# Performance work log

Measured on AMD Instinct MI355X. Metric: run time of the kernel, lower is better.

Reference implementation:

```python
import jax, jax.numpy as jnp
import numpy as np

H = 12      # num_attention_heads
D = 768     # hidden_size
DK = D // H # per-head dim


def setup_inputs() -> dict:
    key = jax.random.key(0)
    ks = jax.random.split(key, 8)
    B, S = 2, 4096
    scale = 0.02
    return {
        "query": jax.random.normal(ks[0], (B, S, D), jnp.float32),
        "key": jax.random.normal(ks[1], (B, S, D), jnp.float32),
        "value": jax.random.normal(ks[2], (B, S, D), jnp.float32),
        "mask": jnp.ones((B, S), jnp.float32),
        "Wq": jax.random.normal(ks[3], (D, D), jnp.float32) * scale,
        "bq": jnp.zeros((D,), jnp.float32),
        "Wk": jax.random.normal(ks[4], (D, D), jnp.float32) * scale,
        "bk": jnp.zeros((D,), jnp.float32),
        "Wv": jax.random.normal(ks[5], (D, D), jnp.float32) * scale,
        "bv": jnp.zeros((D,), jnp.float32),
    }


def reference(query, key, value, mask, Wq, bq, Wk, bk, Wv, bv):
    B, Sq, _ = query.shape
    Sk = key.shape[1]
    # attention mask: ones[B,Sq,1] * mask[B,1,Sk] -> [B,Sq,Sk] -> [B,1,Sq,Sk]
    attn_mask = jnp.ones((B, Sq, 1), jnp.float32) * mask[:, None, :]
    adder = (1.0 - attn_mask)[:, None, :, :] * -10000.0

    q = (query @ Wq + bq).reshape(B, Sq, H, DK).transpose(0, 2, 1, 3)  # [B,H,Sq,DK]
    k = (key @ Wk + bk).reshape(B, Sk, H, DK).transpose(0, 2, 1, 3)
    v = (value @ Wv + bv).reshape(B, Sk, H, DK).transpose(0, 2, 1, 3)

    scores = jnp.einsum("bhqd,bhkd->bhqk", q, k) / jnp.sqrt(jnp.float32(DK))
    scores = scores + adder
    probs = jax.nn.softmax(scores, axis=-1)  # dropout inactive (training=False)
    out = jnp.einsum("bhqk,bhkd->bhqd", probs, v)
    return out.transpose(0, 2, 1, 3).reshape(B, Sq, D)
```

## Files before the change

### kernel.cpp

```cpp
#include <hip/hip_runtime.h>
#include <stdint.h>

#define NH 12
#define DMODEL 768
#define HDK 64
#define SEQ 4096
#define NB 2

typedef __attribute__((ext_vector_type(8))) short bf16x8;
typedef __attribute__((ext_vector_type(4))) short s16x4;
typedef __attribute__((ext_vector_type(4))) float f32x4;
typedef __attribute__((ext_vector_type(16))) float f32x16;

#define LOG2E 1.44269504f
#define QSCALE 0.18033688f
#define CSUB 4.0f

__device__ __forceinline__ unsigned short f2bf(float x) {
    union { float f; unsigned u; } v; v.f = x;
    unsigned r = v.u + 0x7FFFu + ((v.u >> 16) & 1u);
    return (unsigned short)(r >> 16);
}

__device__ __forceinline__ unsigned pack2bf(float a, float b) {
    union { float f; unsigned u; } x, y; x.f = a; y.f = b;
    return __builtin_amdgcn_perm(y.u + 0x8000u, x.u + 0x8000u, 0x07060302u);
}

__device__ __forceinline__ unsigned pack2bf_t(float a, float b) {
    union { float f; unsigned u; } x, y; x.f = a; y.f = b;
    return __builtin_amdgcn_perm(y.u, x.u, 0x07060302u);
}

__device__ __forceinline__ void lds_dma16(const void* g, void* l) {
    __builtin_amdgcn_global_load_lds(
        (const __attribute__((address_space(1))) void*)g,
        (__attribute__((address_space(3))) void*)l, 16, 0, 0);
}

__global__ __launch_bounds__(256) void wt_kernel(
    const float* __restrict__ Wq, const float* __restrict__ Wk,
    const float* __restrict__ Wv, unsigned short* __restrict__ Wt) {
    __shared__ float ts[32][33];
    int mat = blockIdx.z;
    const float* W = (mat == 0) ? Wq : ((mat == 1) ? Wk : Wv);
    unsigned short* out = Wt + (size_t)mat * DMODEL * DMODEL;
    int k0 = blockIdx.x * 32;
    int n0 = blockIdx.y * 32;
    int t = threadIdx.x;
    int row = t >> 3, c4 = (t & 7) * 4;
    float4 v = *(const float4*)&W[(size_t)(k0 + row) * DMODEL + n0 + c4];
    ts[row][c4 + 0] = v.x; ts[row][c4 + 1] = v.y;
    ts[row][c4 + 2] = v.z; ts[row][c4 + 3] = v.w;
    __syncthreads();
    s16x4 o;
    o[0] = (short)f2bf(ts[c4 + 0][row]);
    o[1] = (short)f2bf(ts[c4 + 1][row]);
    o[2] = (short)f2bf(ts[c4 + 2][row]);
    o[3] = (short)f2bf(ts[c4 + 3][row]);
    *(s16x4*)&out[(size_t)(n0 + row) * DMODEL + k0 + c4] = o;
}

__global__ __launch_bounds__(256) void qkv_gemm4(
    const float* __restrict__ Aq, const float* __restrict__ Ak,
    const float* __restrict__ Av, const unsigned short* __restrict__ Wt,
    const float* __restrict__ bq, const float* __restrict__ bk,
    const float* __restrict__ bv,
    unsigned short* __restrict__ Qw, unsigned short* __restrict__ Kw,
    unsigned short* __restrict__ Vt) {
    __shared__ float As[128 * 64];
    __shared__ unsigned short Bs[128 * 64];
    int mat = blockIdx.z;
    const float* A = (mat == 0) ? Aq : ((mat == 1) ? Ak : Av);
    const unsigned short* W = Wt + (size_t)mat * DMODEL * DMODEL;
    const float* bias = (mat == 0) ? bq : ((mat == 1) ? bk : bv);
    int m0 = blockIdx.x * 128;
    int n0 = blockIdx.y * 128;
    int tid = threadIdx.x;
    int lane = tid & 63, wv = tid >> 6;
    int wm = (wv & 1) * 64, wn = (wv >> 1) * 64;
    int lm = lane & 15, quad = lane >> 4;

    const float* aS[8];
    float* aD[8];
    #pragma unroll
    for (int i = 0; i < 8; ++i) {
        int g = i * 256 + tid;
        int R = g >> 4, S = g & 15, c = (S & 8) | ((S & 7) ^ (R & 7));
        aS[i] = A + (size_t)(m0 + R) * DMODEL + c * 4;
        aD[i] = &As[(i * 256 + wv * 64) * 4];
    }
    const unsigned short* bS[4];
    unsigned short* bD[4];
    #pragma unroll
    for (int i = 0; i < 4; ++i) {
        int g = i * 256 + tid;
        int R = g >> 3, S = g & 7, c = S ^ (R & 7);
        bS[i] = W + (size_t)(n0 + R) * DMODEL + c * 8;
        bD[i] = &Bs[(i * 256 + wv * 64) * 8];
    }

    f32x4 acc[4][4] = {};
    int sx = lm & 7;
    const bool swapC = (mat < 2);
    for (int kt = 0; kt < 12; ++kt) {
        __syncthreads();
        #pragma unroll
        for (int i = 0; i < 8; ++i) lds_dma16(aS[i], aD[i]);
        #pragma unroll
        for (int i = 0; i < 4; ++i) lds_dma16(bS[i], bD[i]);
        #pragma unroll
        for (int i = 0; i < 8; ++i) aS[i] += 64;
        #pragma unroll
        for (int i = 0; i < 4; ++i) bS[i] += 64;
        __syncthreads();
        #pragma unroll
        for (int ks = 0; ks < 2; ++ks) {
            bf16x8 af[4], bfr[4];
            #pragma unroll
            for (int i = 0; i < 4; ++i) {
                int r = wm + i * 16 + lm;
                int c0 = ks * 8 + quad * 2;
                int s0 = (c0 & 8) | ((c0 & 7) ^ sx);
                int s1 = (c0 & 8) | (((c0 + 1) & 7) ^ sx);
                f32x4 lo = *(const f32x4*)&As[r * 64 + s0 * 4];
                f32x4 hi = *(const f32x4*)&As[r * 64 + s1 * 4];
                unsigned* au = (unsigned*)&af[i];
                au[0] = pack2bf(lo[0], lo[1]);
                au[1] = pack2bf(lo[2], lo[3]);
                au[2] = pack2bf(hi[0], hi[1]);
                au[3] = pack2bf(hi[2], hi[3]);
            }
            #pragma unroll
            for (int j = 0; j < 4; ++j)
                bfr[j] = *(const bf16x8*)&Bs[(wn + j * 16 + lm) * 64 +
                                             (((ks * 4 + quad) ^ sx) << 3)];
            if (swapC) {
                #pragma unroll
                for (int i = 0; i < 4; ++i)
                    #pragma unroll
                    for (int j = 0; j < 4; ++j)
                        acc[i][j] = __builtin_amdgcn_mfma_f32_16x16x32_bf16(
                            bfr[j], af[i], acc[i][j], 0, 0, 0);
            } else {
                #pragma unroll
                for (int i = 0; i < 4; ++i)
                    #pragma unroll
                    for (int j = 0; j < 4; ++j)
                        acc[i][j] = __builtin_amdgcn_mfma_f32_16x16x32_bf16(
                            af[i], bfr[j], acc[i][j], 0, 0, 0);
            }
        }
    }
    if (swapC) {
        float sc = (mat == 0) ? QSCALE : 1.0f;
        unsigned short* outp = (mat == 0) ? Qw : Kw;
        #pragma unroll
        for (int j = 0; j < 4; ++j) {
            int nbase = n0 + wn + j * 16 + quad * 4;
            f32x4 bvv = *(const f32x4*)&bias[nbase];
            int h = nbase >> 6, dk = nbase & 63;
            #pragma unroll
            for (int i = 0; i < 4; ++i) {
                int s = m0 + wm + i * 16 + lm;
                int b = s >> 12, ss = s & 4095;
                s16x4 o;
                #pragma unroll
                for (int r = 0; r < 4; ++r)
                    o[r] = (short)f2bf((acc[i][j][r] + bvv[r]) * sc);
                *(s16x4*)&outp[((size_t)(b * NH + h) * SEQ + ss) * HDK + dk] = o;
            }
        }
    } else {
        #pragma unroll
        for (int j = 0; j < 4; ++j) {
            int n = n0 + wn + j * 16 + lm;
            float bvv = bias[n];
            int h = n >> 6, dk = n & 63;
            #pragma unroll
            for (int i = 0; i < 4; ++i) {
                int mg = m0 + wm + i * 16 + quad * 4;
                int b = mg >> 12, s = mg & 4095;
                s16x4 o;
                #pragma unroll
                for (int r = 0; r < 4; ++r) o[r] = (short)f2bf(acc[i][j][r] + bvv);
                *(s16x4*)&Vt[((size_t)(b * NH + h) * HDK + dk) * SEQ + s] = o;
            }
        }
    }
}

__global__ __launch_bounds__(256, 3) void attn_kernel(
    const unsigned short* __restrict__ Qw, const unsigned short* __restrict__ Kw,
    const unsigned short* __restrict__ Vt, const float* __restrict__ mask,
    float* __restrict__ out) {
    __shared__ unsigned short Ks[128 * 64];
    __shared__ unsigned short Vs[64 * 128];
    __shared__ float adds[128];

    int q0 = blockIdx.x * 128;
    int bh = blockIdx.y;
    int b = bh / NH, h = bh % NH;
    const unsigned short* Qb = Qw + (size_t)bh * SEQ * HDK;
    const unsigned short* Kb = Kw + (size_t)bh * SEQ * HDK;
    const unsigned short* Vb = Vt + (size_t)bh * HDK * SEQ;
    const float* mb = mask + (size_t)b * SEQ;
    int tid = threadIdx.x;
    int lane = tid & 63, wv = tid >> 6;
    int L31 = lane & 31, hh = lane >> 5;

    int qrow = q0 + wv * 32 + L31;
    bf16x8 qf[4];
    #pragma unroll
    for (int t = 0; t < 4; ++t)
        qf[t] = *(const bf16x8*)&Qb[(size_t)qrow * HDK + t * 16 + hh * 8];

    const unsigned short* kS[4];
    const unsigned short* vS[4];
    unsigned short* kD[4];
    unsigned short* vD[4];
    #pragma unroll
    for (int i = 0; i < 4; ++i) {
        int cc = wv * 4 + i;
        {
            int rho = cc * 8 + (lane >> 3);
            int blk = rho >> 5, c = (rho >> 3) & 3, hb = (rho >> 2) & 1, r2 = rho & 3;
            int kc = blk * 32 + (c & 1) * 16 + hb * 8 + (c >> 1) * 4 + r2;
            int ch = (lane & 7) ^ (rho & 7);
            kS[i] = Kb + (size_t)kc * HDK + ch * 8;
            kD[i] = &Ks[cc * 512];
        }
        {
            int d = cc * 4 + (lane >> 4);
            int c = lane & 15;
            int ch = (c & 8) | ((c & 7) ^ (d & 7));
            vS[i] = Vb + (size_t)d * SEQ + ch * 8;
            vD[i] = &Vs[cc * 512];
        }
    }

    f32x16 Oacc[2] = {};
    f32x16 lacc = {};
    const f32x16 kZero = {};
    bf16x8 ones;
    #pragma unroll
    for (int i = 0; i < 8; ++i) ones[i] = (short)0x3F80;
    const int sx7 = L31 & 7;

    for (int kt = 0; kt < 32; ++kt) {
        __syncthreads();
        #pragma unroll
        for (int i = 0; i < 4; ++i) lds_dma16(kS[i], kD[i]);
        #pragma unroll
        for (int i = 0; i < 4; ++i) lds_dma16(vS[i], vD[i]);
        if (tid < 128)
            adds[tid] = ((1.0f - mb[kt * 128 + tid]) * -10000.0f - CSUB) * LOG2E;
        #pragma unroll
        for (int i = 0; i < 4; ++i) { kS[i] += 128 * HDK; vS[i] += 128; }
        __syncthreads();

        #pragma unroll
        for (int blk = 0; blk < 4; ++blk) {
            f32x16 sacc;
            {
                bf16x8 kf = *(const bf16x8*)&Ks[(blk * 32 + L31) * 64 +
                                                ((hh ^ sx7) << 3)];
                sacc = __builtin_amdgcn_mfma_f32_32x32x16_bf16(kf, qf[0], kZero, 0, 0, 0);
            }
            #pragma unroll
            for (int t = 1; t < 4; ++t) {
                bf16x8 kf = *(const bf16x8*)&Ks[(blk * 32 + L31) * 64 +
                                                (((2 * t + hh) ^ sx7) << 3)];
                sacc = __builtin_amdgcn_mfma_f32_32x32x16_bf16(kf, qf[t], sacc, 0, 0, 0);
            }

            unsigned pkk[2][4];
            #pragma unroll
            for (int c2 = 0; c2 < 4; ++c2) {
                f32x4 adv = *(const f32x4*)&adds[blk * 32 + (c2 & 1) * 16 +
                                                 (c2 >> 1) * 4 + hh * 8];
                float p0 = __builtin_amdgcn_exp2f(sacc[c2 * 4 + 0] + adv[0]);
                float p1 = __builtin_amdgcn_exp2f(sacc[c2 * 4 + 1] + adv[1]);
                float p2 = __builtin_amdgcn_exp2f(sacc[c2 * 4 + 2] + adv[2]);
                float p3 = __builtin_amdgcn_exp2f(sacc[c2 * 4 + 3] + adv[3]);
                pkk[c2 & 1][2 * (c2 >> 1) + 0] = pack2bf_t(p0, p1);
                pkk[c2 & 1][2 * (c2 >> 1) + 1] = pack2bf_t(p2, p3);
            }

            #pragma unroll
            for (int kbi = 0; kbi < 2; ++kbi) {
                bf16x8 pf;
                unsigned* pu = (unsigned*)&pf;
                pu[0] = pkk[kbi][0]; pu[1] = pkk[kbi][1];
                pu[2] = pkk[kbi][2]; pu[3] = pkk[kbi][3];
                int kb = blk * 2 + kbi;
                lacc = __builtin_amdgcn_mfma_f32_32x32x16_bf16(ones, pf, lacc, 0, 0, 0);
                #pragma unroll
                for (int dj = 0; dj < 2; ++dj) {
                    int c = kb * 2 + hh;
                    int slot = (c & 8) | ((c & 7) ^ (lane & 7));
                    bf16x8 vf = *(const bf16x8*)&Vs[(dj * 32 + L31) * 128 + slot * 8];
                    Oacc[dj] = __builtin_amdgcn_mfma_f32_32x32x16_bf16(vf, pf, Oacc[dj], 0, 0, 0);
                }
            }
        }
    }

    float rl = 1.0f / lacc[0];
    size_t base = ((size_t)b * SEQ + qrow) * DMODEL + h * HDK;
    #pragma unroll
    for (int dj = 0; dj < 2; ++dj)
        #pragma unroll
        for (int c2 = 0; c2 < 4; ++c2) {
            int d = dj * 32 + 8 * c2 + 4 * hh;
            float4 o;
            o.x = Oacc[dj][c2 * 4 + 0] * rl;
            o.y = Oacc[dj][c2 * 4 + 1] * rl;
            o.z = Oacc[dj][c2 * 4 + 2] * rl;
            o.w = Oacc[dj][c2 * 4 + 3] * rl;
            *(float4*)&out[base + d] = o;
        }
}

extern "C" void kernel_launch(void* const* d_in, const int* in_sizes, int n_in,
                              void* d_out, int out_size, void* d_ws, size_t ws_size,
                              hipStream_t stream) {
    (void)in_sizes; (void)n_in; (void)out_size; (void)ws_size;
    const float* query = (const float*)d_in[0];
    const float* key   = (const float*)d_in[1];
    const float* value = (const float*)d_in[2];
    const float* mask  = (const float*)d_in[3];
    const float* Wq    = (const float*)d_in[4];
    const float* bq    = (const float*)d_in[5];
    const float* Wk    = (const float*)d_in[6];
    const float* bk    = (const float*)d_in[7];
    const float* Wv    = (const float*)d_in[8];
    const float* bv    = (const float*)d_in[9];

    const size_t WT_BYTES  = (size_t)3 * DMODEL * DMODEL * 2;
    const size_t QKV_BYTES = (size_t)NB * NH * SEQ * HDK * 2;
    unsigned short* Wt = (unsigned short*)d_ws;
    unsigned short* Qw = (unsigned short*)((char*)d_ws + WT_BYTES);
    unsigned short* Kw = (unsigned short*)((char*)d_ws + WT_BYTES + QKV_BYTES);
    unsigned short* Vt = (unsigned short*)((char*)d_ws + WT_BYTES + 2 * QKV_BYTES);

    wt_kernel<<<dim3(24, 24, 3), 256, 0, stream>>>(Wq, Wk, Wv, Wt);
    qkv_gemm4<<<dim3(64, 6, 3), 256, 0, stream>>>(query, key, value, Wt,
                                                  bq, bk, bv, Qw, Kw, Vt);
    attn_kernel<<<dim3(32, 24), 256, 0, stream>>>(Qw, Kw, Vt, mask, (float*)d_out);
}
```

Measured before the change: 308.3 us.

## Restructure attention to 2-wave blocks with double-buffered K and swizzled grids

The attention kernel now uses 128-thread blocks where each wave handles 64 query rows as two 32-row tiles, sharing each K/V LDS fragment across two MFMA streams. K tiles are double-buffered so the next tile's DMA overlaps the current compute, with explicit waitcnt, barriers, sched_barrier and setprio around MFMA bursts. The row-sum is computed with scalar adds plus a cross-half shuffle instead of a ones-matrix MFMA. Both the GEMM and attention grids become 1D with an XCD-aware block swizzle. Risks include higher register pressure, lower occupancy from 2-wave blocks, and fragile hand-written vmcnt counts.

```diff
diff --git a/kernel.cpp b/kernel.cpp
--- a/kernel.cpp
+++ b/kernel.cpp
@@ -15,6 +15,8 @@
 #define LOG2E 1.44269504f
 #define QSCALE 0.18033688f
 #define CSUB 4.0f
+
+#define SBAR() __builtin_amdgcn_sched_barrier(0)
 
 __device__ __forceinline__ unsigned short f2bf(float x) {
     union { float f; unsigned u; } v; v.f = x;
@@ -70,12 +72,17 @@
     unsigned short* __restrict__ Vt) {
     __shared__ float As[128 * 64];
     __shared__ unsigned short Bs[128 * 64];
-    int mat = blockIdx.z;
+    int lin = blockIdx.x;
+    int swz = (lin & 7) * 144 + (lin >> 3);
+    int mat = swz / 384;
+    int rr = swz - mat * 384;
+    int mblk = rr / 6;
+    int nblk = rr - mblk * 6;
     const float* A = (mat == 0) ? Aq : ((mat == 1) ? Ak : Av);
     const unsigned short* W = Wt + (size_t)mat * DMODEL * DMODEL;
     const float* bias = (mat == 0) ? bq : ((mat == 1) ? bk : bv);
-    int m0 = blockIdx.x * 128;
-    int n0 = blockIdx.y * 128;
+    int m0 = mblk * 128;
+    int n0 = nblk * 128;
     int tid = threadIdx.x;
     int lane = tid & 63, wv = tid >> 6;
     int wm = (wv & 1) * 64, wn = (wv >> 1) * 64;
@@ -190,16 +197,18 @@
     }
 }
 
-__global__ __launch_bounds__(256, 3) void attn_kernel(
+__global__ __launch_bounds__(128, 2) void attn_kernel(
     const unsigned short* __restrict__ Qw, const unsigned short* __restrict__ Kw,
     const unsigned short* __restrict__ Vt, const float* __restrict__ mask,
     float* __restrict__ out) {
-    __shared__ unsigned short Ks[128 * 64];
+    __shared__ unsigned short Ks[2][128 * 64];
     __shared__ unsigned short Vs[64 * 128];
     __shared__ float adds[128];
 
-    int q0 = blockIdx.x * 128;
-    int bh = blockIdx.y;
+    int lin = blockIdx.x;
+    int swz = (lin & 7) * 96 + (lin >> 3);
+    int q0 = (swz & 31) * 128;
+    int bh = swz >> 5;
     int b = bh / NH, h = bh % NH;
     const unsigned short* Qb = Qw + (size_t)bh * SEQ * HDK;
     const unsigned short* Kb = Kw + (size_t)bh * SEQ * HDK;
@@ -208,117 +217,167 @@
     int tid = threadIdx.x;
     int lane = tid & 63, wv = tid >> 6;
     int L31 = lane & 31, hh = lane >> 5;
-
-    int qrow = q0 + wv * 32 + L31;
-    bf16x8 qf[4];
-    #pragma unroll
-    for (int t = 0; t < 4; ++t)
-        qf[t] = *(const bf16x8*)&Qb[(size_t)qrow * HDK + t * 16 + hh * 8];
-
-    const unsigned short* kS[4];
-    const unsigned short* vS[4];
-    unsigned short* kD[4];
-    unsigned short* vD[4];
-    #pragma unroll
-    for (int i = 0; i < 4; ++i) {
-        int cc = wv * 4 + i;
+    const int sx7 = L31 & 7;
+
+    int qrow = q0 + wv * 64 + L31;
+    bf16x8 qa[4], qbv[4];
+    #pragma unroll
+    for (int t = 0; t < 4; ++t) {
+        qa[t] = *(const bf16x8*)&Qb[(size_t)qrow * HDK + t * 16 + hh * 8];
+        qbv[t] = *(const bf16x8*)&Qb[(size_t)(qrow + 32) * HDK + t * 16 + hh * 8];
+    }
+    asm volatile("s_waitcnt vmcnt(0)" ::: "memory");
+
+    const unsigned short* kS[8];
+    const unsigned short* vS[8];
+    #pragma unroll
+    for (int i = 0; i < 8; ++i) {
+        int cc = wv * 8 + i;
         {
             int rho = cc * 8 + (lane >> 3);
             int blk = rho >> 5, c = (rho >> 3) & 3, hb = (rho >> 2) & 1, r2 = rho & 3;
             int kc = blk * 32 + (c & 1) * 16 + hb * 8 + (c >> 1) * 4 + r2;
             int ch = (lane & 7) ^ (rho & 7);
             kS[i] = Kb + (size_t)kc * HDK + ch * 8;
-            kD[i] = &Ks[cc * 512];
         }
         {
             int d = cc * 4 + (lane >> 4);
             int c = lane & 15;
             int ch = (c & 8) | ((c & 7) ^ (d & 7));
             vS[i] = Vb + (size_t)d * SEQ + ch * 8;
-            vD[i] = &Vs[cc * 512];
-        }
-    }
-
-    f32x16 Oacc[2] = {};
-    f32x16 lacc = {};
+        }
+    }
+    #pragma unroll
+    for (int i = 0; i < 8; ++i) {
+        lds_dma16(kS[i], &Ks[0][(wv * 8 + i) * 512]);
+        kS[i] += 128 * HDK;
+    }
+    SBAR();
+
+    f32x16 Oa[2] = {}, Ob[2] = {};
+    float lpa = 0.0f, lpb = 0.0f;
     const f32x16 kZero = {};
-    bf16x8 ones;
-    #pragma unroll
-    for (int i = 0; i < 8; ++i) ones[i] = (short)0x3F80;
-    const int sx7 = L31 & 7;
 
     for (int kt = 0; kt < 32; ++kt) {
-        __syncthreads();
-        #pragma unroll
-        for (int i = 0; i < 4; ++i) lds_dma16(kS[i], kD[i]);
-        #pragma unroll
-        for (int i = 0; i < 4; ++i) lds_dma16(vS[i], vD[i]);
-        if (tid < 128)
-            adds[tid] = ((1.0f - mb[kt * 128 + tid]) * -10000.0f - CSUB) * LOG2E;
-        #pragma unroll
-        for (int i = 0; i < 4; ++i) { kS[i] += 128 * HDK; vS[i] += 128; }
-        __syncthreads();
+        int cur = kt & 1;
+        const unsigned short* Kc = &Ks[cur][0];
+        SBAR();
+        __builtin_amdgcn_s_barrier();
+        SBAR();
+        float mbv = mb[kt * 128 + tid];
+        adds[tid] = ((1.0f - mbv) * -10000.0f - CSUB) * LOG2E;
+        SBAR();
+        #pragma unroll
+        for (int i = 0; i < 8; ++i) {
+            lds_dma16(vS[i], &Vs[(wv * 8 + i) * 512]);
+            vS[i] += 128;
+        }
+        if (kt < 31) {
+            unsigned short* kn = &Ks[cur ^ 1][0];
+            #pragma unroll
+            for (int i = 0; i < 8; ++i) {
+                lds_dma16(kS[i], kn + (wv * 8 + i) * 512);
+                kS[i] += 128 * HDK;
+            }
+        }
+        SBAR();
+        asm volatile("s_waitcnt lgkmcnt(0)" ::: "memory");
+        __builtin_amdgcn_s_barrier();
+        SBAR();
 
         #pragma unroll
         for (int blk = 0; blk < 4; ++blk) {
-            f32x16 sacc;
+            f32x16 sa, sb;
+            __builtin_amdgcn_s_setprio(1);
             {
-                bf16x8 kf = *(const bf16x8*)&Ks[(blk * 32 + L31) * 64 +
+                bf16x8 kf = *(const bf16x8*)&Kc[(blk * 32 + L31) * 64 +
                                                 ((hh ^ sx7) << 3)];
-                sacc = __builtin_amdgcn_mfma_f32_32x32x16_bf16(kf, qf[0], kZero, 0, 0, 0);
+                sa = __builtin_amdgcn_mfma_f32_32x32x16_bf16(kf, qa[0], kZero, 0, 0, 0);
+                sb = __builtin_amdgcn_mfma_f32_32x32x16_bf16(kf, qbv[0], kZero, 0, 0, 0);
             }
             #pragma unroll
             for (int t = 1; t < 4; ++t) {
-                bf16x8 kf = *(const bf16x8*)&Ks[(blk * 32 + L31) * 64 +
+                bf16x8 kf = *(const bf16x8*)&Kc[(blk * 32 + L31) * 64 +
                                                 (((2 * t + hh) ^ sx7) << 3)];
-                sacc = __builtin_amdgcn_mfma_f32_32x32x16_bf16(kf, qf[t], sacc, 0, 0, 0);
-            }
-
-            unsigned pkk[2][4];
+                sa = __builtin_amdgcn_mfma_f32_32x32x16_bf16(kf, qa[t], sa, 0, 0, 0);
+                sb = __builtin_amdgcn_mfma_f32_32x32x16_bf16(kf, qbv[t], sb, 0, 0, 0);
+            }
+            __builtin_amdgcn_s_setprio(0);
+
+            unsigned pkkA[2][4], pkkB[2][4];
             #pragma unroll
             for (int c2 = 0; c2 < 4; ++c2) {
                 f32x4 adv = *(const f32x4*)&adds[blk * 32 + (c2 & 1) * 16 +
                                                  (c2 >> 1) * 4 + hh * 8];
-                float p0 = __builtin_amdgcn_exp2f(sacc[c2 * 4 + 0] + adv[0]);
-                float p1 = __builtin_amdgcn_exp2f(sacc[c2 * 4 + 1] + adv[1]);
-                float p2 = __builtin_amdgcn_exp2f(sacc[c2 * 4 + 2] + adv[2]);
-                float p3 = __builtin_amdgcn_exp2f(sacc[c2 * 4 + 3] + adv[3]);
-                pkk[c2 & 1][2 * (c2 >> 1) + 0] = pack2bf_t(p0, p1);
-                pkk[c2 & 1][2 * (c2 >> 1) + 1] = pack2bf_t(p2, p3);
-            }
-
+                float a0 = __builtin_amdgcn_exp2f(sa[c2 * 4 + 0] + adv[0]);
+                float a1 = __builtin_amdgcn_exp2f(sa[c2 * 4 + 1] + adv[1]);
+                float a2 = __builtin_amdgcn_exp2f(sa[c2 * 4 + 2] + adv[2]);
+                float a3 = __builtin_amdgcn_exp2f(sa[c2 * 4 + 3] + adv[3]);
+                lpa += (a0 + a1) + (a2 + a3);
+                pkkA[c2 & 1][2 * (c2 >> 1) + 0] = pack2bf_t(a0, a1);
+                pkkA[c2 & 1][2 * (c2 >> 1) + 1] = pack2bf_t(a2, a3);
+                float b0 = __builtin_amdgcn_exp2f(sb[c2 * 4 + 0] + adv[0]);
+                float b1 = __builtin_amdgcn_exp2f(sb[c2 * 4 + 1] + adv[1]);
+                float b2 = __builtin_amdgcn_exp2f(sb[c2 * 4 + 2] + adv[2]);
+                float b3 = __builtin_amdgcn_exp2f(sb[c2 * 4 + 3] + adv[3]);
+                lpb += (b0 + b1) + (b2 + b3);
+                pkkB[c2 & 1][2 * (c2 >> 1) + 0] = pack2bf_t(b0, b1);
+                pkkB[c2 & 1][2 * (c2 >> 1) + 1] = pack2bf_t(b2, b3);
+            }
+
+            if (blk == 0) {
+                SBAR();
+                if (kt < 31) asm volatile("s_waitcnt vmcnt(8)" ::: "memory");
+                else         asm volatile("s_waitcnt vmcnt(0)" ::: "memory");
+                __builtin_amdgcn_s_barrier();
+                SBAR();
+            }
+
+            __builtin_amdgcn_s_setprio(1);
             #pragma unroll
             for (int kbi = 0; kbi < 2; ++kbi) {
-                bf16x8 pf;
-                unsigned* pu = (unsigned*)&pf;
-                pu[0] = pkk[kbi][0]; pu[1] = pkk[kbi][1];
-                pu[2] = pkk[kbi][2]; pu[3] = pkk[kbi][3];
-                int kb = blk * 2 + kbi;
-                lacc = __builtin_amdgcn_mfma_f32_32x32x16_bf16(ones, pf, lacc, 0, 0, 0);
+                bf16x8 pfA, pfB;
+                unsigned* pa = (unsigned*)&pfA;
+                unsigned* pb = (unsigned*)&pfB;
+                pa[0] = pkkA[kbi][0]; pa[1] = pkkA[kbi][1];
+                pa[2] = pkkA[kbi][2]; pa[3] = pkkA[kbi][3];
+                pb[0] = pkkB[kbi][0]; pb[1] = pkkB[kbi][1];
+                pb[2] = pkkB[kbi][2]; pb[3] = pkkB[kbi][3];
                 #pragma unroll
                 for (int dj = 0; dj < 2; ++dj) {
-                    int c = kb * 2 + hh;
+                    int c = (blk * 2 + kbi) * 2 + hh;
                     int slot = (c & 8) | ((c & 7) ^ (lane & 7));
                     bf16x8 vf = *(const bf16x8*)&Vs[(dj * 32 + L31) * 128 + slot * 8];
-                    Oacc[dj] = __builtin_amdgcn_mfma_f32_32x32x16_bf16(vf, pf, Oacc[dj], 0, 0, 0);
+                    Oa[dj] = __builtin_amdgcn_mfma_f32_32x32x16_bf16(vf, pfA, Oa[dj], 0, 0, 0);
+                    Ob[dj] = __builtin_amdgcn_mfma_f32_32x32x16_bf16(vf, pfB, Ob[dj], 0, 0, 0);
                 }
             }
-        }
-    }
-
-    float rl = 1.0f / lacc[0];
-    size_t base = ((size_t)b * SEQ + qrow) * DMODEL + h * HDK;
+            __builtin_amdgcn_s_setprio(0);
+        }
+    }
+
+    lpa += __shfl_xor(lpa, 32);
+    lpb += __shfl_xor(lpb, 32);
+    float rla = 1.0f / lpa;
+    float rlb = 1.0f / lpb;
+    size_t basea = ((size_t)b * SEQ + qrow) * DMODEL + h * HDK;
     #pragma unroll
     for (int dj = 0; dj < 2; ++dj)
         #pragma unroll
         for (int c2 = 0; c2 < 4; ++c2) {
             int d = dj * 32 + 8 * c2 + 4 * hh;
             float4 o;
-            o.x = Oacc[dj][c2 * 4 + 0] * rl;
-            o.y = Oacc[dj][c2 * 4 + 1] * rl;
-            o.z = Oacc[dj][c2 * 4 + 2] * rl;
-            o.w = Oacc[dj][c2 * 4 + 3] * rl;
-            *(float4*)&out[base + d] = o;
+            o.x = Oa[dj][c2 * 4 + 0] * rla;
+            o.y = Oa[dj][c2 * 4 + 1] * rla;
+            o.z = Oa[dj][c2 * 4 + 2] * rla;
+            o.w = Oa[dj][c2 * 4 + 3] * rla;
+            *(float4*)&out[basea + d] = o;
+            float4 o2;
+            o2.x = Ob[dj][c2 * 4 + 0] * rlb;
+            o2.y = Ob[dj][c2 * 4 + 1] * rlb;
+            o2.z = Ob[dj][c2 * 4 + 2] * rlb;
+            o2.w = Ob[dj][c2 * 4 + 3] * rlb;
+            *(float4*)&out[basea + (size_t)32 * DMODEL + d] = o2;
         }
 }
 
@@ -345,7 +404,7 @@
     unsigned short* Vt = (unsigned short*)((char*)d_ws + WT_BYTES + 2 * QKV_BYTES);
 
     wt_kernel<<<dim3(24, 24, 3), 256, 0, stream>>>(Wq, Wk, Wv, Wt);
-    qkv_gemm4<<<dim3(64, 6, 3), 256, 0, stream>>>(query, key, value, Wt,
-                                                  bq, bk, bv, Qw, Kw, Vt);
-    attn_kernel<<<dim3(32, 24), 256, 0, stream>>>(Qw, Kw, Vt, mask, (float*)d_out);
-}
+    qkv_gemm4<<<dim3(1152), 256, 0, stream>>>(query, key, value, Wt,
+                                              bq, bk, bv, Qw, Kw, Vt);
+    attn_kernel<<<dim3(768), 128, 0, stream>>>(Qw, Kw, Vt, mask, (float*)d_out);
+}
```

Measured after the change: 502.6 us. +63.0%, slower.
